# Performance work log

Hardware: AMD Instinct MI355X
Metric: run time of the kernel (lower is better)

Reference implementation:

```python
import jax, jax.numpy as jnp
import numpy as np

N_NODES = 100000
N_EDGES = 3200000
N_FEAT = 128
HIDDEN = 16
MLP_H = 100
N_CLASSES = 12
N_GRAPHS = 512


def setup_inputs() -> dict:
    key = jax.random.key(0)
    ks = jax.random.split(key, 12)
    x = jax.random.normal(ks[0], (N_NODES, N_FEAT), dtype=jnp.float32)
    edge_index = jax.random.randint(ks[1], (2, N_EDGES), 0, N_NODES, dtype=jnp.int64)
    batch_vec = jnp.sort(jax.random.randint(ks[2], (N_NODES,), 0, N_GRAPHS, dtype=jnp.int64))
    def glorot(k, shape):
        lim = np.sqrt(6.0 / (shape[0] + shape[1]))
        return jax.random.uniform(k, shape, jnp.float32, -lim, lim)
    W1 = glorot(ks[3], (N_FEAT, HIDDEN)); b1 = jnp.zeros((HIDDEN,), jnp.float32)
    W2 = glorot(ks[4], (HIDDEN, HIDDEN)); b2 = jnp.zeros((HIDDEN,), jnp.float32)
    lw1 = glorot(ks[5], (HIDDEN, MLP_H)); lb1 = jnp.zeros((MLP_H,), jnp.float32)
    lw2 = glorot(ks[6], (MLP_H, N_CLASSES)); lb2 = jnp.zeros((N_CLASSES,), jnp.float32)
    return {"x": x, "edge_index": edge_index, "batch_vec": batch_vec,
            "W1": W1, "b1": b1, "W2": W2, "b2": b2,
            "lw1": lw1, "lb1": lb1, "lw2": lw2, "lb2": lb2}


def _gcn_edges(edge_index):
    # add self loops, compute symmetric normalization (PyG GCNConv default)
    loop = jnp.arange(N_NODES, dtype=edge_index.dtype)
    src = jnp.concatenate([edge_index[0], loop])
    dst = jnp.concatenate([edge_index[1], loop])
    deg = jax.ops.segment_sum(jnp.ones_like(dst, dtype=jnp.float32), dst,
                              num_segments=N_NODES)
    dinv = jnp.where(deg > 0, jax.lax.rsqrt(deg), 0.0)
    norm = dinv[src] * dinv[dst]  # [E+N]
    return src, dst, norm


def _gcn_conv(x, W, b, src, dst, norm):
    h = x @ W                                # [N, out]
    msg = h[src] * norm[:, None]             # gather + scale, [E+N, out]
    out = jax.ops.segment_sum(msg, dst, num_segments=N_NODES)
    return out + b


def reference(x, edge_index, batch_vec, W1, b1, W2, b2, lw1, lb1, lw2, lb2):
    src, dst, norm = _gcn_edges(edge_index)
    h = jax.nn.relu(_gcn_conv(x, W1, b1, src, dst, norm))   # dropout: eval no-op
    h = _gcn_conv(h, W2, b2, src, dst, norm)
    h = jax.nn.relu(h)
    pooled = jax.ops.segment_sum(h, batch_vec, num_segments=N_GRAPHS)  # global_add_pool
    g = jax.nn.relu(pooled)
    g = jax.nn.relu(g @ lw1 + lb1)
    return g @ lw2 + lb2  # [N_GRAPHS, N_CLASSES] logits
```

## Files before the change

kernel.cpp:

```cpp
#include <hip/hip_runtime.h>

#define N_NODES   100000
#define N_EDGES   3200000
#define N_FEAT    128
#define HIDDEN    16
#define MLP_H     100
#define N_CLASSES 12
#define N_GRAPHS  512
#define BNODES    512
#define NBUCK     196
#define BCAP      18400
#define CPAD      16
#define RING      64
#define BIN_BLOCKS 256
#define GEMM_BLOCKS 391

__global__ __launch_bounds__(256) void kInit(int* __restrict__ gcursor,
                                             float* __restrict__ pooled) {
    int t = blockIdx.x * 256 + threadIdx.x;
    if (t < NBUCK) gcursor[t * CPAD] = t * BCAP;
    if (t < N_GRAPHS * HIDDEN) pooled[t] = 0.f;
}

__global__ __launch_bounds__(256) void kBinGemm(const int* __restrict__ src,
                                                const int* __restrict__ dst,
                                                int* __restrict__ gcursor,
                                                int* __restrict__ pairs,
                                                const float* __restrict__ x,
                                                const float* __restrict__ W1,
                                                float* __restrict__ hp) {
    __shared__ union {
        struct { int ring[NBUCK * RING]; int cnt[NBUCK]; int fl[NBUCK]; } bin;
        float gw[N_FEAT * HIDDEN];
    } sm;
    int t = threadIdx.x;
    if (blockIdx.x < BIN_BLOCKS) {
        for (int i = t; i < NBUCK; i += 256) { sm.bin.cnt[i] = 0; sm.bin.fl[i] = 0; }
        __syncthreads();
        const int batch = 256 * 8;
        for (int base = blockIdx.x * batch; base < N_EDGES;
             base += BIN_BLOCKS * batch) {
            int e0 = base + t * 8;
            if (e0 < N_EDGES) {
                int4 d4a = *(const int4*)&dst[e0];
                int4 d4b = *(const int4*)&dst[e0 + 4];
                int4 s4a = *(const int4*)&src[e0];
                int4 s4b = *(const int4*)&src[e0 + 4];
                int dd[8] = {d4a.x, d4a.y, d4a.z, d4a.w,
                             d4b.x, d4b.y, d4b.z, d4b.w};
                int ss[8] = {s4a.x, s4a.y, s4a.z, s4a.w,
                             s4b.x, s4b.y, s4b.z, s4b.w};
#pragma unroll
                for (int k = 0; k < 8; ++k) {
                    int b = dd[k] >> 9;
                    int p = atomicAdd(&sm.bin.cnt[b], 1);
                    sm.bin.ring[b * RING + (p & (RING - 1))] =
                        (ss[k] << 9) | (dd[k] & 511);
                }
            }
            __syncthreads();
            if (t < NBUCK) {
                while (sm.bin.cnt[t] - sm.bin.fl[t] >= 16) {
                    int start = sm.bin.fl[t];
                    int gpos = atomicAdd(&gcursor[t * CPAD], 16);
                    int rbase = t * RING + (start & (RING - 1));
                    const int4* rp = (const int4*)&sm.bin.ring[rbase];
                    int4* gp = (int4*)&pairs[gpos];
                    gp[0] = rp[0]; gp[1] = rp[1]; gp[2] = rp[2]; gp[3] = rp[3];
                    sm.bin.fl[t] = start + 16;
                }
            }
            __syncthreads();
        }
        if (t < NBUCK) {
            int pending = sm.bin.cnt[t] - sm.bin.fl[t];
            if (pending > 0) {
                int gpos = atomicAdd(&gcursor[t * CPAD], pending);
                for (int k = 0; k < pending; ++k)
                    pairs[gpos + k] =
                        sm.bin.ring[t * RING + ((sm.bin.fl[t] + k) & (RING - 1))];
            }
        }
    } else {
        for (int i = t; i < N_FEAT * HIDDEN; i += 256) sm.gw[i] = W1[i];
        __syncthreads();
        int n = (blockIdx.x - BIN_BLOCKS) * 256 + t;
        if (n >= N_NODES) return;
        float acc[HIDDEN];
#pragma unroll
        for (int j = 0; j < HIDDEN; ++j) acc[j] = 0.f;
        const float4* xr = (const float4*)(x + (size_t)n * N_FEAT);
#pragma unroll 4
        for (int k4 = 0; k4 < N_FEAT / 4; ++k4) {
            float4 v = xr[k4];
            float xk[4] = {v.x, v.y, v.z, v.w};
#pragma unroll
            for (int kk = 0; kk < 4; ++kk) {
                const float4* wrow = (const float4*)&sm.gw[(k4 * 4 + kk) * HIDDEN];
#pragma unroll
                for (int j4 = 0; j4 < 4; ++j4) {
                    float4 wv = wrow[j4];
                    acc[j4 * 4 + 0] += xk[kk] * wv.x;
                    acc[j4 * 4 + 1] += xk[kk] * wv.y;
                    acc[j4 * 4 + 2] += xk[kk] * wv.z;
                    acc[j4 * 4 + 3] += xk[kk] * wv.w;
                }
            }
        }
        float4* hr = (float4*)(hp + (size_t)n * HIDDEN);
#pragma unroll
        for (int j4 = 0; j4 < 4; ++j4)
            hr[j4] = make_float4(acc[j4 * 4 + 0], acc[j4 * 4 + 1],
                                 acc[j4 * 4 + 2], acc[j4 * 4 + 3]);
    }
}

__global__ __launch_bounds__(512) void kBuild(const int* __restrict__ gcursor,
                                              int* __restrict__ pairs,
                                              int2* __restrict__ odc,
                                              float* __restrict__ hp) {
    __shared__ int lp[BCAP];
    __shared__ int hist[BNODES];
    __shared__ int sc[BNODES];
    __shared__ int lcur[BNODES];
    __shared__ float dvl[BNODES];
    int b = blockIdx.x, t = threadIdx.x;
    int base = b * BCAP;
    int cnt = gcursor[b * CPAD] - base;
    for (int i = t; i < cnt; i += 512) lp[i] = pairs[base + i];
    hist[t] = 0;
    __syncthreads();
    for (int i = t; i < cnt; i += 512) atomicAdd(&hist[lp[i] & 511], 1);
    __syncthreads();
    int deg = hist[t];
    int deg4 = (deg + 3) & ~3;
    sc[t] = deg4;
    __syncthreads();
    for (int s = 1; s < 512; s <<= 1) {
        int a = (t >= s) ? sc[t - s] : 0;
        __syncthreads();
        sc[t] += a;
        __syncthreads();
    }
    int g = b * BNODES + t;
    int excl = base + sc[t] - deg4;
    lcur[t] = excl;
    dvl[t] = rsqrtf((float)deg + 1.0f);
    if (g < N_NODES) odc[g] = make_int2(excl, deg);
    __syncthreads();
    for (int i = t; i < cnt; i += 512) {
        int v = lp[i];
        int pos = atomicAdd(&lcur[v & 511], 1);
        pairs[pos] = (v >> 9) << 6;
    }
    for (int p = deg; p < deg4; ++p) pairs[excl + p] = -16;
    __syncthreads();
    int fbase = b * BNODES * HIDDEN;
#pragma unroll
    for (int i = 0; i < 16; ++i) {
        int f = i * 512 + t;
        int gi = fbase + f;
        if (gi < N_NODES * HIDDEN) hp[gi] *= dvl[f >> 4];
    }
}

template <int MODE>
__global__ __launch_bounds__(256)
void kAgg(const float* __restrict__ hp, const int2* __restrict__ odc,
          const int* __restrict__ csr, const float* __restrict__ W2,
          const float* __restrict__ bias, float* __restrict__ outbuf,
          const int* __restrict__ batch, float* __restrict__ pooled) {
    __shared__ float W2s[HIDDEN * HIDDEN];
    __shared__ float bs[HIDDEN];
    __shared__ float red[256];
    __shared__ int sseg[2];
    int t = threadIdx.x;
    if (MODE == 1) W2s[t] = W2[t];
    if (t < HIDDEN) bs[t] = bias[t];
    int n0 = blockIdx.x * 16;
    if (MODE == 0) {
        if (t == 0) sseg[0] = batch[n0];
        if (t == 1) sseg[1] = batch[n0 + 15];
    }
    __syncthreads();

    int gid = blockIdx.x * 256 + t;
    int n = gid >> 4;
    int l16 = gid & 15;
    int jj = l16 & 3;
    int eq = l16 >> 2;
    int2 oc = odc[n];
    int beg = oc.x, deg = oc.y;
    int deg4 = (deg + 3) & ~3;
    const char* hpc = (const char*)hp;
    const int4* csr4 = (const int4*)csr;
    int c4 = (beg >> 2) + eq;
    int jb = jj << 4;
    float4 a4 = make_float4(0.f, 0.f, 0.f, 0.f);

    int4 i4 = (eq * 4 < deg4) ? csr4[c4] : make_int4(-16, -16, -16, -16);
    for (int cur = 0; cur < deg4; cur += 16) {
        int nxt = cur + 16;
        int4 p4 = (nxt + eq * 4 < deg4) ? csr4[c4 + (nxt >> 2)]
                                        : make_int4(-16, -16, -16, -16);
        float4 v0 = (i4.x >= 0) ? *(const float4*)(hpc + i4.x + jb)
                                : make_float4(0.f, 0.f, 0.f, 0.f);
        float4 v1 = (i4.y >= 0) ? *(const float4*)(hpc + i4.y + jb)
                                : make_float4(0.f, 0.f, 0.f, 0.f);
        float4 v2 = (i4.z >= 0) ? *(const float4*)(hpc + i4.z + jb)
                                : make_float4(0.f, 0.f, 0.f, 0.f);
        float4 v3 = (i4.w >= 0) ? *(const float4*)(hpc + i4.w + jb)
                                : make_float4(0.f, 0.f, 0.f, 0.f);
        a4.x += v0.x + v1.x + v2.x + v3.x;
        a4.y += v0.y + v1.y + v2.y + v3.y;
        a4.z += v0.z + v1.z + v2.z + v3.z;
        a4.w += v0.w + v1.w + v2.w + v3.w;
        i4 = p4;
    }
    a4.x += __shfl_xor(a4.x, 4, 16);  a4.y += __shfl_xor(a4.y, 4, 16);
    a4.z += __shfl_xor(a4.z, 4, 16);  a4.w += __shfl_xor(a4.w, 4, 16);
    a4.x += __shfl_xor(a4.x, 8, 16);  a4.y += __shfl_xor(a4.y, 8, 16);
    a4.z += __shfl_xor(a4.z, 8, 16);  a4.w += __shfl_xor(a4.w, 8, 16);
    int srcl = l16 >> 2;
    float c0 = __shfl(a4.x, srcl, 16);
    float c1 = __shfl(a4.y, srcl, 16);
    float c2 = __shfl(a4.z, srcl, 16);
    float c3 = __shfl(a4.w, srcl, 16);
    int cc = l16 & 3;
    float acc = (cc == 0) ? c0 : (cc == 1) ? c1 : (cc == 2) ? c2 : c3;
    acc += hp[(size_t)n * HIDDEN + l16];
    float dv = rsqrtf((float)deg + 1.0f);
    if (MODE == 1) {
        float tt = fmaxf(acc * dv + bs[l16], 0.f);
        float o = 0.f;
#pragma unroll
        for (int k = 0; k < 16; ++k)
            o += __shfl(tt, k, 16) * W2s[k * HIDDEN + l16];
        outbuf[(size_t)n * HIDDEN + l16] = o * dv;
    } else {
        float val = fmaxf(acc * dv + bs[l16], 0.f);
        int ln = t >> 4;
        red[t] = val;
        __syncthreads();
        if (sseg[0] == sseg[1]) {
            if (ln < 8) red[t] += red[t + 128];
            __syncthreads();
            if (ln < 4) red[t] += red[t + 64];
            __syncthreads();
            if (ln < 2) red[t] += red[t + 32];
            __syncthreads();
            if (ln == 0)
                unsafeAtomicAdd(&pooled[(size_t)sseg[0] * HIDDEN + l16],
                                red[t] + red[t + 16]);
        } else {
            unsafeAtomicAdd(&pooled[(size_t)batch[n] * HIDDEN + l16], val);
        }
    }
}

__global__ __launch_bounds__(64) void kMlp(const float* __restrict__ pooled,
                                           const float* __restrict__ lw1,
                                           const float* __restrict__ lb1,
                                           const float* __restrict__ lw2,
                                           const float* __restrict__ lb2,
                                           float* __restrict__ out) {
    int g = blockIdx.x * 64 + threadIdx.x;
    if (g >= N_GRAPHS) return;
    float gv[HIDDEN];
#pragma unroll
    for (int k = 0; k < HIDDEN; ++k)
        gv[k] = fmaxf(pooled[(size_t)g * HIDDEN + k], 0.f);
    float o[N_CLASSES];
#pragma unroll
    for (int c = 0; c < N_CLASSES; ++c) o[c] = lb2[c];
    for (int j = 0; j < MLP_H; ++j) {
        float s = lb1[j];
#pragma unroll
        for (int k = 0; k < HIDDEN; ++k) s += gv[k] * lw1[k * MLP_H + j];
        s = fmaxf(s, 0.f);
#pragma unroll
        for (int c = 0; c < N_CLASSES; ++c) o[c] += s * lw2[j * N_CLASSES + c];
    }
#pragma unroll
    for (int c = 0; c < N_CLASSES; ++c) out[(size_t)g * N_CLASSES + c] = o[c];
}

extern "C" void kernel_launch(void* const* d_in, const int* in_sizes, int n_in,
                              void* d_out, int out_size, void* d_ws,
                              size_t ws_size, hipStream_t stream) {
    const float* x     = (const float*)d_in[0];
    const int*   ei    = (const int*)d_in[1];
    const int*   batch = (const int*)d_in[2];
    const float* W1    = (const float*)d_in[3];
    const float* b1    = (const float*)d_in[4];
    const float* W2    = (const float*)d_in[5];
    const float* b2    = (const float*)d_in[6];
    const float* lw1   = (const float*)d_in[7];
    const float* lb1   = (const float*)d_in[8];
    const float* lw2   = (const float*)d_in[9];
    const float* lb2   = (const float*)d_in[10];
    float* out = (float*)d_out;

    const int* src = ei;
    const int* dst = ei + N_EDGES;

    char*  ws      = (char*)d_ws;
    int*   gcursor = (int*)(ws + 0);
    int2*  odc     = (int2*)(ws + 16384);
    int*   pairs   = (int*)(ws + 816384);
    float* hp      = (float*)(ws + 15241984);
    float* hp2     = (float*)(ws + 21641984);
    float* pooled  = (float*)(ws + 28041984);

    kInit<<<32, 256, 0, stream>>>(gcursor, pooled);
    kBinGemm<<<BIN_BLOCKS + GEMM_BLOCKS, 256, 0, stream>>>(
        src, dst, gcursor, pairs, x, W1, hp);
    kBuild<<<NBUCK, 512, 0, stream>>>(gcursor, pairs, odc, hp);
    kAgg<1><<<N_NODES / 16, 256, 0, stream>>>(hp, odc, pairs, W2, b1, hp2,
                                              nullptr, nullptr);
    kAgg<0><<<N_NODES / 16, 256, 0, stream>>>(hp2, odc, pairs, nullptr, b2,
                                              nullptr, batch, pooled);
    kMlp<<<(N_GRAPHS + 63) / 64, 64, 0, stream>>>(pooled, lw1, lb1, lw2, lb2, out);
}
```

Measured before the change: 163.8 us.

## Store node feature tables in fp16 to halve gather traffic in aggregation

Node features are now written as half precision: the first GEMM's output, the degree-scaled copy and the layer-2 transformed features. Each neighbor gather in the aggregation kernels loads 8 bytes per lane instead of 16 and accumulates in fp32. Column indices are rescaled to the new row stride and loaded with nontemporal hints. The binning ring shrinks from 64 to 48 entries per bucket, which needs modulo indexing and cuts LDS use. Storing activations in fp16 adds rounding error on the hidden features.

```diff
diff --git a/kernel.cpp b/kernel.cpp
--- a/kernel.cpp
+++ b/kernel.cpp
@@ -1,4 +1,5 @@
 #include <hip/hip_runtime.h>
+#include <hip/hip_fp16.h>
 
 #define N_NODES   100000
 #define N_EDGES   3200000
@@ -11,9 +12,11 @@
 #define NBUCK     196
 #define BCAP      18400
 #define CPAD      16
-#define RING      64
+#define RING      48
 #define BIN_BLOCKS 256
 #define GEMM_BLOCKS 391
+
+typedef int vint4 __attribute__((ext_vector_type(4)));
 
 __global__ __launch_bounds__(256) void kInit(int* __restrict__ gcursor,
                                              float* __restrict__ pooled) {
@@ -28,7 +31,7 @@
                                                 int* __restrict__ pairs,
                                                 const float* __restrict__ x,
                                                 const float* __restrict__ W1,
-                                                float* __restrict__ hp) {
+                                                __half* __restrict__ hp16) {
     __shared__ union {
         struct { int ring[NBUCK * RING]; int cnt[NBUCK]; int fl[NBUCK]; } bin;
         float gw[N_FEAT * HIDDEN];
@@ -54,7 +57,7 @@
                 for (int k = 0; k < 8; ++k) {
                     int b = dd[k] >> 9;
                     int p = atomicAdd(&sm.bin.cnt[b], 1);
-                    sm.bin.ring[b * RING + (p & (RING - 1))] =
+                    sm.bin.ring[b * RING + (p % RING)] =
                         (ss[k] << 9) | (dd[k] & 511);
                 }
             }
@@ -63,7 +66,7 @@
                 while (sm.bin.cnt[t] - sm.bin.fl[t] >= 16) {
                     int start = sm.bin.fl[t];
                     int gpos = atomicAdd(&gcursor[t * CPAD], 16);
-                    int rbase = t * RING + (start & (RING - 1));
+                    int rbase = t * RING + (start % RING);
                     const int4* rp = (const int4*)&sm.bin.ring[rbase];
                     int4* gp = (int4*)&pairs[gpos];
                     gp[0] = rp[0]; gp[1] = rp[1]; gp[2] = rp[2]; gp[3] = rp[3];
@@ -78,7 +81,7 @@
                 int gpos = atomicAdd(&gcursor[t * CPAD], pending);
                 for (int k = 0; k < pending; ++k)
                     pairs[gpos + k] =
-                        sm.bin.ring[t * RING + ((sm.bin.fl[t] + k) & (RING - 1))];
+                        sm.bin.ring[t * RING + ((sm.bin.fl[t] + k) % RING)];
             }
         }
     } else {
@@ -107,18 +110,20 @@
                 }
             }
         }
-        float4* hr = (float4*)(hp + (size_t)n * HIDDEN);
-#pragma unroll
-        for (int j4 = 0; j4 < 4; ++j4)
-            hr[j4] = make_float4(acc[j4 * 4 + 0], acc[j4 * 4 + 1],
-                                 acc[j4 * 4 + 2], acc[j4 * 4 + 3]);
+        union { __half2 h2[8]; int4 v4[2]; } u;
+#pragma unroll
+        for (int j2 = 0; j2 < 8; ++j2)
+            u.h2[j2] = __floats2half2_rn(acc[2 * j2], acc[2 * j2 + 1]);
+        int4* hr = (int4*)(hp16 + (size_t)n * HIDDEN);
+        hr[0] = u.v4[0];
+        hr[1] = u.v4[1];
     }
 }
 
 __global__ __launch_bounds__(512) void kBuild(const int* __restrict__ gcursor,
                                               int* __restrict__ pairs,
                                               int2* __restrict__ odc,
-                                              float* __restrict__ hp) {
+                                              __half2* __restrict__ hp2p) {
     __shared__ int lp[BCAP];
     __shared__ int hist[BNODES];
     __shared__ int sc[BNODES];
@@ -151,24 +156,28 @@
     for (int i = t; i < cnt; i += 512) {
         int v = lp[i];
         int pos = atomicAdd(&lcur[v & 511], 1);
-        pairs[pos] = (v >> 9) << 6;
+        pairs[pos] = (v >> 9) << 5;
     }
     for (int p = deg; p < deg4; ++p) pairs[excl + p] = -16;
     __syncthreads();
-    int fbase = b * BNODES * HIDDEN;
-#pragma unroll
-    for (int i = 0; i < 16; ++i) {
+    int hbase = b * BNODES * 8;
+#pragma unroll
+    for (int i = 0; i < 8; ++i) {
         int f = i * 512 + t;
-        int gi = fbase + f;
-        if (gi < N_NODES * HIDDEN) hp[gi] *= dvl[f >> 4];
+        int g2 = hbase + f;
+        if (g2 < N_NODES * 8) {
+            float d = dvl[f >> 3];
+            float2 ff = __half22float2(hp2p[g2]);
+            hp2p[g2] = __floats2half2_rn(ff.x * d, ff.y * d);
+        }
     }
 }
 
 template <int MODE>
 __global__ __launch_bounds__(256)
-void kAgg(const float* __restrict__ hp, const int2* __restrict__ odc,
+void kAgg(const __half* __restrict__ hp, const int2* __restrict__ odc,
           const int* __restrict__ csr, const float* __restrict__ W2,
-          const float* __restrict__ bias, float* __restrict__ outbuf,
+          const float* __restrict__ bias, __half* __restrict__ out16,
           const int* __restrict__ batch, float* __restrict__ pooled) {
     __shared__ float W2s[HIDDEN * HIDDEN];
     __shared__ float bs[HIDDEN];
@@ -193,28 +202,30 @@
     int beg = oc.x, deg = oc.y;
     int deg4 = (deg + 3) & ~3;
     const char* hpc = (const char*)hp;
-    const int4* csr4 = (const int4*)csr;
+    const vint4* csr4 = (const vint4*)csr;
     int c4 = (beg >> 2) + eq;
-    int jb = jj << 4;
+    int jb = jj << 3;
     float4 a4 = make_float4(0.f, 0.f, 0.f, 0.f);
-
-    int4 i4 = (eq * 4 < deg4) ? csr4[c4] : make_int4(-16, -16, -16, -16);
+    const vint4 msent = {-16, -16, -16, -16};
+    const uint2 z2 = make_uint2(0u, 0u);
+
+    vint4 i4 = (eq * 4 < deg4) ? __builtin_nontemporal_load(&csr4[c4]) : msent;
     for (int cur = 0; cur < deg4; cur += 16) {
         int nxt = cur + 16;
-        int4 p4 = (nxt + eq * 4 < deg4) ? csr4[c4 + (nxt >> 2)]
-                                        : make_int4(-16, -16, -16, -16);
-        float4 v0 = (i4.x >= 0) ? *(const float4*)(hpc + i4.x + jb)
-                                : make_float4(0.f, 0.f, 0.f, 0.f);
-        float4 v1 = (i4.y >= 0) ? *(const float4*)(hpc + i4.y + jb)
-                                : make_float4(0.f, 0.f, 0.f, 0.f);
-        float4 v2 = (i4.z >= 0) ? *(const float4*)(hpc + i4.z + jb)
-                                : make_float4(0.f, 0.f, 0.f, 0.f);
-        float4 v3 = (i4.w >= 0) ? *(const float4*)(hpc + i4.w + jb)
-                                : make_float4(0.f, 0.f, 0.f, 0.f);
-        a4.x += v0.x + v1.x + v2.x + v3.x;
-        a4.y += v0.y + v1.y + v2.y + v3.y;
-        a4.z += v0.z + v1.z + v2.z + v3.z;
-        a4.w += v0.w + v1.w + v2.w + v3.w;
+        vint4 p4 = (nxt + eq * 4 < deg4)
+                       ? __builtin_nontemporal_load(&csr4[c4 + (nxt >> 2)])
+                       : msent;
+        uint2 u0 = (i4.x >= 0) ? *(const uint2*)(hpc + i4.x + jb) : z2;
+        uint2 u1 = (i4.y >= 0) ? *(const uint2*)(hpc + i4.y + jb) : z2;
+        uint2 u2 = (i4.z >= 0) ? *(const uint2*)(hpc + i4.z + jb) : z2;
+        uint2 u3 = (i4.w >= 0) ? *(const uint2*)(hpc + i4.w + jb) : z2;
+#pragma unroll
+        for (int q = 0; q < 4; ++q) {
+            uint2 u = (q == 0) ? u0 : (q == 1) ? u1 : (q == 2) ? u2 : u3;
+            float2 lo = __half22float2(*(const __half2*)&u.x);
+            float2 hi = __half22float2(*(const __half2*)&u.y);
+            a4.x += lo.x; a4.y += lo.y; a4.z += hi.x; a4.w += hi.y;
+        }
         i4 = p4;
     }
     a4.x += __shfl_xor(a4.x, 4, 16);  a4.y += __shfl_xor(a4.y, 4, 16);
@@ -228,7 +239,7 @@
     float c3 = __shfl(a4.w, srcl, 16);
     int cc = l16 & 3;
     float acc = (cc == 0) ? c0 : (cc == 1) ? c1 : (cc == 2) ? c2 : c3;
-    acc += hp[(size_t)n * HIDDEN + l16];
+    acc += __half2float(hp[(size_t)n * HIDDEN + l16]);
     float dv = rsqrtf((float)deg + 1.0f);
     if (MODE == 1) {
         float tt = fmaxf(acc * dv + bs[l16], 0.f);
@@ -236,7 +247,10 @@
 #pragma unroll
         for (int k = 0; k < 16; ++k)
             o += __shfl(tt, k, 16) * W2s[k * HIDDEN + l16];
-        outbuf[(size_t)n * HIDDEN + l16] = o * dv;
+        float od = o * dv;
+        float on = __shfl_xor(od, 1, 16);
+        if (!(l16 & 1))
+            ((__half2*)out16)[n * 8 + (l16 >> 1)] = __floats2half2_rn(od, on);
     } else {
         float val = fmaxf(acc * dv + bs[l16], 0.f);
         int ln = t >> 4;
@@ -304,21 +318,21 @@
     const int* src = ei;
     const int* dst = ei + N_EDGES;
 
-    char*  ws      = (char*)d_ws;
-    int*   gcursor = (int*)(ws + 0);
-    int2*  odc     = (int2*)(ws + 16384);
-    int*   pairs   = (int*)(ws + 816384);
-    float* hp      = (float*)(ws + 15241984);
-    float* hp2     = (float*)(ws + 21641984);
-    float* pooled  = (float*)(ws + 28041984);
+    char*   ws      = (char*)d_ws;
+    int*    gcursor = (int*)(ws + 0);
+    int2*   odc     = (int2*)(ws + 16384);
+    int*    pairs   = (int*)(ws + 816384);
+    __half* hp16    = (__half*)(ws + 15241984);
+    __half* hp2_16  = (__half*)(ws + 18441984);
+    float*  pooled  = (float*)(ws + 21641984);
 
     kInit<<<32, 256, 0, stream>>>(gcursor, pooled);
     kBinGemm<<<BIN_BLOCKS + GEMM_BLOCKS, 256, 0, stream>>>(
-        src, dst, gcursor, pairs, x, W1, hp);
-    kBuild<<<NBUCK, 512, 0, stream>>>(gcursor, pairs, odc, hp);
-    kAgg<1><<<N_NODES / 16, 256, 0, stream>>>(hp, odc, pairs, W2, b1, hp2,
-                                              nullptr, nullptr);
-    kAgg<0><<<N_NODES / 16, 256, 0, stream>>>(hp2, odc, pairs, nullptr, b2,
+        src, dst, gcursor, pairs, x, W1, hp16);
+    kBuild<<<NBUCK, 512, 0, stream>>>(gcursor, pairs, odc, (__half2*)hp16);
+    kAgg<1><<<N_NODES / 16, 256, 0, stream>>>(hp16, odc, pairs, W2, b1,
+                                              hp2_16, nullptr, nullptr);
+    kAgg<0><<<N_NODES / 16, 256, 0, stream>>>(hp2_16, odc, pairs, nullptr, b2,
                                               nullptr, batch, pooled);
     kMlp<<<(N_GRAPHS + 63) / 64, 64, 0, stream>>>(pooled, lw1, lb1, lw2, lb2, out);
 }
```

Result: slower. 180.1 us (+10.0%).
